# Performance work log

Hardware: AMD Instinct MI355X
Metric: run time of the kernel (lower is better)

The kernel has to match this reference:

```python
import jax, jax.numpy as jnp
import numpy as np

D_MODEL = 1024
N_HEADS = 16
D_K = D_MODEL // N_HEADS
B, S = 4, 2048


def setup_inputs() -> dict:
    key = jax.random.key(0)
    ks = jax.random.split(key, 12)
    scale = 1.0 / np.sqrt(D_MODEL)
    mk = lambda k: (jax.random.uniform(k, (D_MODEL, D_MODEL), jnp.float32, -scale, scale))
    mb = lambda k: (jax.random.uniform(k, (D_MODEL,), jnp.float32, -scale, scale))
    mask = jnp.tril(jnp.ones((S, S), dtype=bool))[None, None, :, :]  # [1,1,S,S] causal
    return {
        "query": jax.random.normal(ks[0], (B, S, D_MODEL), jnp.float32),
        "key": jax.random.normal(ks[1], (B, S, D_MODEL), jnp.float32),
        "value": jax.random.normal(ks[2], (B, S, D_MODEL), jnp.float32),
        "w_q": mk(ks[3]), "b_q": mb(ks[4]),
        "w_k": mk(ks[5]), "b_k": mb(ks[6]),
        "w_v": mk(ks[7]), "b_v": mb(ks[8]),
        "w_o": mk(ks[9]), "b_o": mb(ks[10]),
        "mask": mask,
    }


def _split_heads(x):
    b, s, _ = x.shape
    return x.reshape(b, s, N_HEADS, D_K).transpose(0, 2, 1, 3)  # [B,H,S,Dk]


def reference(query, key, value, w_q, b_q, w_k, b_k, w_v, b_v, w_o, b_o, mask):
    Q = _split_heads(query @ w_q.T + b_q)
    K = _split_heads(key @ w_k.T + b_k)
    V = _split_heads(value @ w_v.T + b_v)
    scores = jnp.einsum("bhqd,bhkd->bhqk", Q, K) / jnp.sqrt(jnp.asarray(D_K, Q.dtype))
    min_val = jnp.finfo(scores.dtype).min
    scores = jnp.where(mask, scores, min_val)
    attn = jax.nn.softmax(scores, axis=-1)
    ctx = jnp.einsum("bhqk,bhkd->bhqd", attn, V)
    ctx = ctx.transpose(0, 2, 1, 3).reshape(query.shape[0], -1, D_MODEL)
    return ctx @ w_o.T + b_o
```

## Files before the change

### kernel.cpp

```cpp
#include <hip/hip_runtime.h>
#include <cstdint>
#include <cstddef>

#define DM 1024
#define NH 16
#define DK 64
#define BB 4
#define SS 2048
#define MROWS (BB*SS)

#define NE_ ((size_t)MROWS * DM)
#define WE_ ((size_t)DM * DM)

typedef __attribute__((ext_vector_type(8))) __bf16 bf16x8;
typedef __attribute__((ext_vector_type(4))) float f32x4;
typedef __attribute__((ext_vector_type(8))) unsigned short ushort8;

#define SCALE_LOG2E 0.18033688011112042f

__device__ __forceinline__ unsigned short f2bf(float f) {
  union { float f; unsigned u; } v; v.f = f;
  unsigned r = v.u + 0x7fffu + ((v.u >> 16) & 1u);
  return (unsigned short)(r >> 16);
}

__device__ __forceinline__ unsigned short f2bf_hw(float f) {
  __bf16 h = (__bf16)f;
  return __builtin_bit_cast(unsigned short, h);
}

__device__ __forceinline__ void async_load16(const void* g, void* l) {
  __builtin_amdgcn_global_load_lds(
      (__attribute__((address_space(1))) void*)(g),
      (__attribute__((address_space(3))) void*)(l),
      16, 0, 0);
}

template<int CTRL>
__device__ __forceinline__ float dppf(float v) {
  int i = __builtin_bit_cast(int, v);
  int r = __builtin_amdgcn_update_dpp(i, i, CTRL, 0xf, 0xf, true);
  return __builtin_bit_cast(float, r);
}
__device__ __forceinline__ float redsum16(float v) {
  v += dppf<0x128>(v);
  v += dppf<0x124>(v);
  v += dppf<0x122>(v);
  v += dppf<0x121>(v);
  return v;
}

struct CvtArgs {
  const float* src[7];
  unsigned short* dst[7];
};

__global__ __launch_bounds__(256)
void cvt_all(CvtArgs a) {
  size_t i = ((size_t)blockIdx.x * 256 + threadIdx.x) * 4;
  int seg; size_t off;
  if (i < 3 * NE_) { seg = (int)(i >> 23); off = i & (NE_ - 1); }
  else { size_t j = i - 3 * NE_; seg = 3 + (int)(j >> 20); off = j & (WE_ - 1); }
  float4 v = *reinterpret_cast<const float4*>(a.src[seg] + off);
  ushort4 o;
  o.x = f2bf(v.x); o.y = f2bf(v.y); o.z = f2bf(v.z); o.w = f2bf(v.w);
  *reinterpret_cast<ushort4*>(a.dst[seg] + off) = o;
}

struct QkvArgs {
  const unsigned short* A[3];
  const unsigned short* W[3];
  const float* bias[3];
  unsigned short* out[3];
};

__global__ __launch_bounds__(256)
void gemm_qkv(QkvArgs qa)
{
  __shared__ __align__(16) unsigned short As[128*32];
  __shared__ __align__(16) unsigned short Bs[128*32];

  const int sel = blockIdx.x >> 3;
  const unsigned short* __restrict__ A  = qa.A[sel];
  const unsigned short* __restrict__ Bw = qa.W[sel];
  const float* __restrict__ bias = qa.bias[sel];
  unsigned short* __restrict__ o = qa.out[sel];
  const float qs = (sel == 0) ? SCALE_LOG2E : 1.0f;

  const int tid  = threadIdx.x;
  const int lane = tid & 63;
  const int wv   = tid >> 6;
  const int wm   = wv >> 1, wn = wv & 1;
  const int gm0  = blockIdx.y * 128;
  const int gn0  = (blockIdx.x & 7) * 128;
  const int lrow = lane & 15;
  const int lk8  = (lane >> 4) * 8;

  f32x4 acc[4][4] = {};

  for (int k0 = 0; k0 < DM; k0 += 32) {
    __syncthreads();
    #pragma unroll
    for (int p = 0; p < 2; ++p) {
      int idx = (p * 256 + tid) * 8;
      int row = idx >> 5;
      int col = idx & 31;
      async_load16(&A [(size_t)(gm0 + row) * DM + k0 + col], &As[idx]);
      async_load16(&Bw[(size_t)(gn0 + row) * DM + k0 + col], &Bs[idx]);
    }
    __syncthreads();

    bf16x8 af[4], bfr[4];
    #pragma unroll
    for (int m = 0; m < 4; ++m)
      af[m] = *reinterpret_cast<const bf16x8*>(&As[(wm*64 + m*16 + lrow)*32 + lk8]);
    #pragma unroll
    for (int n = 0; n < 4; ++n)
      bfr[n] = *reinterpret_cast<const bf16x8*>(&Bs[(wn*64 + n*16 + lrow)*32 + lk8]);
    #pragma unroll
    for (int m = 0; m < 4; ++m)
      #pragma unroll
      for (int n = 0; n < 4; ++n)
        acc[m][n] = __builtin_amdgcn_mfma_f32_16x16x32_bf16(af[m], bfr[n], acc[m][n], 0, 0, 0);
  }

  const int orow = (lane >> 4) * 4;
  const int ocol = lane & 15;
  #pragma unroll
  for (int n = 0; n < 4; ++n) {
    int gn = gn0 + wn*64 + n*16 + ocol;
    float bv = bias[gn] * qs;
    int h = gn >> 6, d = gn & (DK - 1);
    #pragma unroll
    for (int m = 0; m < 4; ++m) {
      #pragma unroll
      for (int r = 0; r < 4; ++r) {
        int gm = gm0 + wm*64 + m*16 + orow + r;
        int b = gm >> 11, s = gm & (SS - 1);
        o[(((size_t)b*NH + h)*SS + s)*DK + d] = f2bf_hw(fmaf(acc[m][n][r], qs, bv));
      }
    }
  }
}

__global__ __launch_bounds__(256)
void gemm_out(const unsigned short* __restrict__ A,
              const unsigned short* __restrict__ Bw,
              const float* __restrict__ bias,
              float* __restrict__ o)
{
  __shared__ __align__(16) unsigned short As[128*32];
  __shared__ __align__(16) unsigned short Bs[128*32];

  const int tid  = threadIdx.x;
  const int lane = tid & 63;
  const int wv   = tid >> 6;
  const int wm   = wv >> 1, wn = wv & 1;
  const int gm0  = blockIdx.y * 128;
  const int gn0  = blockIdx.x * 128;
  const int lrow = lane & 15;
  const int lk8  = (lane >> 4) * 8;

  f32x4 acc[4][4] = {};

  for (int k0 = 0; k0 < DM; k0 += 32) {
    __syncthreads();
    #pragma unroll
    for (int p = 0; p < 2; ++p) {
      int idx = (p * 256 + tid) * 8;
      int row = idx >> 5;
      int col = idx & 31;
      async_load16(&A [(size_t)(gm0 + row) * DM + k0 + col], &As[idx]);
      async_load16(&Bw[(size_t)(gn0 + row) * DM + k0 + col], &Bs[idx]);
    }
    __syncthreads();

    bf16x8 af[4], bfr[4];
    #pragma unroll
    for (int m = 0; m < 4; ++m)
      af[m] = *reinterpret_cast<const bf16x8*>(&As[(wm*64 + m*16 + lrow)*32 + lk8]);
    #pragma unroll
    for (int n = 0; n < 4; ++n)
      bfr[n] = *reinterpret_cast<const bf16x8*>(&Bs[(wn*64 + n*16 + lrow)*32 + lk8]);
    #pragma unroll
    for (int m = 0; m < 4; ++m)
      #pragma unroll
      for (int n = 0; n < 4; ++n)
        acc[m][n] = __builtin_amdgcn_mfma_f32_16x16x32_bf16(af[m], bfr[n], acc[m][n], 0, 0, 0);
  }

  const int orow = (lane >> 4) * 4;
  const int ocol = lane & 15;
  #pragma unroll
  for (int n = 0; n < 4; ++n) {
    int gn = gn0 + wn*64 + n*16 + ocol;
    float bv = bias[gn];
    #pragma unroll
    for (int m = 0; m < 4; ++m)
      #pragma unroll
      for (int r = 0; r < 4; ++r) {
        int gm = gm0 + wm*64 + m*16 + orow + r;
        o[(size_t)gm * DM + gn] = acc[m][n][r] + bv;
      }
  }
}

__global__ __launch_bounds__(256)
void vtrans_kernel(const unsigned short* __restrict__ Vp, unsigned short* __restrict__ VpT) {
  __shared__ unsigned short T[64][72];
  const int bh = blockIdx.x;
  const int st = blockIdx.y;
  const int tid = threadIdx.x;
  #pragma unroll
  for (int p = 0; p < 2; ++p) {
    int i = p*256 + tid;
    int row = i >> 3, c8 = (i & 7) * 8;
    *reinterpret_cast<ushort8*>(&T[row][c8]) =
      *reinterpret_cast<const ushort8*>(&Vp[((size_t)bh*SS + st*64 + row)*DK + c8]);
  }
  __syncthreads();
  #pragma unroll
  for (int p = 0; p < 2; ++p) {
    int i = p*256 + tid;
    int d = i >> 3, s8 = (i & 7) * 8;
    ushort8 o;
    #pragma unroll
    for (int j = 0; j < 8; ++j) o[j] = T[s8 + j][d];
    *reinterpret_cast<ushort8*>(&VpT[((size_t)bh*DK + d)*SS + st*64 + s8]) = o;
  }
}

__global__ __launch_bounds__(512)
void attn_kernel(const unsigned short* __restrict__ Qp,
                 const unsigned short* __restrict__ Kp,
                 const unsigned short* __restrict__ VpT,
                 unsigned short* __restrict__ ctx)
{
  __shared__ __align__(16) unsigned short Kb[2][64*64];
  __shared__ __align__(16) unsigned short Vb[2][64*64];
  __shared__ __align__(16) unsigned short Ps[8][16][72];

  const int tid  = threadIdx.x;
  const int lane = tid & 63;
  const int w    = tid >> 6;
  const int bh   = blockIdx.x;
  const int qt   = gridDim.y - 1 - blockIdx.y;
  const int qb0  = qt * 128;
  const int qw0  = qb0 + w * 16;
  const int lrow = lane & 15;
  const int g0   = lane >> 4;
  const int lk8  = g0 * 8;

  const size_t qbase = ((size_t)bh * SS + qw0 + lrow) * DK;
  bf16x8 aq0 = *reinterpret_cast<const bf16x8*>(&Qp[qbase + lk8]);
  bf16x8 aq1 = *reinterpret_cast<const bf16x8*>(&Qp[qbase + 32 + lk8]);

  f32x4 accc[4] = {};
  float psum[4] = {0.f, 0.f, 0.f, 0.f};

  const int ntiles = 2*qt + 2;
  const int twlast = (qw0 + 15) >> 6;
  const int srow   = tid >> 3;
  const int ssrc   = (tid & 7) ^ (srow & 7);

#define STAGE(B, T) { \
    const int kv0_ = (T) * 64; \
    async_load16(&Kp [((size_t)bh*SS + kv0_ + srow)*DK + ssrc*8], &Kb[B][tid*8]); \
    async_load16(&VpT[((size_t)bh*DK + srow)*SS + kv0_ + ssrc*8], &Vb[B][tid*8]); }

  STAGE(0, 0);

  for (int t = 0; t < ntiles; ++t) {
    const int buf = t & 1;
    asm volatile("s_waitcnt vmcnt(0)" ::: "memory");
    __syncthreads();
    if (t + 1 < ntiles) { if (buf) { STAGE(0, t + 1); } else { STAGE(1, t + 1); } }

    if (t <= twlast) {
      const int kv0 = t * 64;
      const unsigned short* Kc = &Kb[buf][0];
      const unsigned short* Vc = &Vb[buf][0];

      f32x4 sc[4];
      __builtin_amdgcn_s_setprio(1);
      #pragma unroll
      for (int kb = 0; kb < 4; ++kb) {
        const int rk = kb*16 + lrow;
        const int cx = rk & 7;
        bf16x8 bk0 = *reinterpret_cast<const bf16x8*>(&Kc[rk*64 + ((g0    ) ^ cx)*8]);
        bf16x8 bk1 = *reinterpret_cast<const bf16x8*>(&Kc[rk*64 + ((g0 + 4) ^ cx)*8]);
        f32x4 z = {};
        z      = __builtin_amdgcn_mfma_f32_16x16x32_bf16(aq0, bk0, z, 0, 0, 0);
        sc[kb] = __builtin_amdgcn_mfma_f32_16x16x32_bf16(aq1, bk1, z, 0, 0, 0);
      }
      __builtin_amdgcn_s_setprio(0);

      const int qrow0 = qw0 + g0 * 4;
      const bool needmask = (kv0 + 63 > qw0);
      #pragma unroll
      for (int kb = 0; kb < 4; ++kb) {
        const int kvg = kv0 + kb*16 + lrow;
        #pragma unroll
        for (int r = 0; r < 4; ++r) {
          float p = __builtin_amdgcn_exp2f(sc[kb][r]);
          if (needmask && (kvg > qrow0 + r)) p = 0.f;
          sc[kb][r] = p;
          psum[r] += p;
        }
      }

      #pragma unroll
      for (int kb = 0; kb < 4; ++kb)
        #pragma unroll
        for (int r = 0; r < 4; ++r)
          Ps[w][g0*4 + r][kb*16 + lrow] = f2bf_hw(sc[kb][r]);
      asm volatile("s_waitcnt lgkmcnt(0)" ::: "memory");

      bf16x8 pa0 = *reinterpret_cast<const bf16x8*>(&Ps[w][lrow][lk8]);
      bf16x8 pa1 = *reinterpret_cast<const bf16x8*>(&Ps[w][lrow][32 + lk8]);
      __builtin_amdgcn_s_setprio(1);
      #pragma unroll
      for (int db = 0; db < 4; ++db) {
        const int rv = db*16 + lrow;
        const int cv = rv & 7;
        bf16x8 bv0 = *reinterpret_cast<const bf16x8*>(&Vc[rv*64 + ((g0    ) ^ cv)*8]);
        bf16x8 bv1 = *reinterpret_cast<const bf16x8*>(&Vc[rv*64 + ((g0 + 4) ^ cv)*8]);
        accc[db] = __builtin_amdgcn_mfma_f32_16x16x32_bf16(pa0, bv0, accc[db], 0, 0, 0);
        accc[db] = __builtin_amdgcn_mfma_f32_16x16x32_bf16(pa1, bv1, accc[db], 0, 0, 0);
      }
      __builtin_amdgcn_s_setprio(0);
    }
  }

  const int b = bh >> 4, hh = bh & (NH - 1);
  #pragma unroll
  for (int r = 0; r < 4; ++r) {
    int q = qw0 + g0*4 + r;
    float l = redsum16(psum[r]);
    float inv = __builtin_amdgcn_rcpf(l);
    size_t base = ((size_t)b * SS + q) * DM + hh * DK;
    #pragma unroll
    for (int db = 0; db < 4; ++db)
      ctx[base + db*16 + lrow] = f2bf_hw(accc[db][r] * inv);
  }
}

extern "C" void kernel_launch(void* const* d_in, const int* in_sizes, int n_in,
                              void* d_out, int out_size, void* d_ws, size_t ws_size,
                              hipStream_t stream)
{
  const float* q_in = (const float*)d_in[0];
  const float* k_in = (const float*)d_in[1];
  const float* v_in = (const float*)d_in[2];
  const float* w_q  = (const float*)d_in[3];
  const float* b_q  = (const float*)d_in[4];
  const float* w_k  = (const float*)d_in[5];
  const float* b_k  = (const float*)d_in[6];
  const float* w_v  = (const float*)d_in[7];
  const float* b_v  = (const float*)d_in[8];
  const float* w_o  = (const float*)d_in[9];
  const float* b_o  = (const float*)d_in[10];

  char* ws = (char*)d_ws;
  size_t off = 0;
  unsigned short* xb[3];
  unsigned short* wb[4];
  for (int i = 0; i < 3; ++i) { xb[i] = (unsigned short*)(ws + off); off += NE_ * 2; }
  for (int i = 0; i < 4; ++i) { wb[i] = (unsigned short*)(ws + off); off += WE_ * 2; }
  unsigned short* Qp  = (unsigned short*)(ws + off); off += NE_ * 2;
  unsigned short* Kp  = (unsigned short*)(ws + off); off += NE_ * 2;
  unsigned short* Vp  = (unsigned short*)(ws + off); off += NE_ * 2;
  unsigned short* ctx = (unsigned short*)(ws + off); off += NE_ * 2;
  unsigned short* VpT = xb[2];

  CvtArgs ca;
  ca.src[0] = q_in; ca.dst[0] = xb[0];
  ca.src[1] = k_in; ca.dst[1] = xb[1];
  ca.src[2] = v_in; ca.dst[2] = xb[2];
  ca.src[3] = w_q;  ca.dst[3] = wb[0];
  ca.src[4] = w_k;  ca.dst[4] = wb[1];
  ca.src[5] = w_v;  ca.dst[5] = wb[2];
  ca.src[6] = w_o;  ca.dst[6] = wb[3];
  const int cvt_blocks = (int)((3*NE_ + 4*WE_) / 1024);
  cvt_all<<<cvt_blocks, 256, 0, stream>>>(ca);

  QkvArgs qa;
  qa.A[0] = xb[0]; qa.W[0] = wb[0]; qa.bias[0] = b_q; qa.out[0] = Qp;
  qa.A[1] = xb[1]; qa.W[1] = wb[1]; qa.bias[1] = b_k; qa.out[1] = Kp;
  qa.A[2] = xb[2]; qa.W[2] = wb[2]; qa.bias[2] = b_v; qa.out[2] = Vp;
  gemm_qkv<<<dim3(24, MROWS/128), 256, 0, stream>>>(qa);

  vtrans_kernel<<<dim3(BB*NH, SS/64), 256, 0, stream>>>(Vp, VpT);

  attn_kernel<<<dim3(BB*NH, SS/128), 512, 0, stream>>>(Qp, Kp, VpT, ctx);

  gemm_out<<<dim3(DM/128, MROWS/128), 256, 0, stream>>>(ctx, wb[3], b_o, (float*)d_out);
}
```

Baseline: 200.4 us.

## Double-buffer GEMM LDS tiles, remap workgroups for XCD locality, raise MFMA priority

Both projection GEMMs now use two LDS buffers per operand, so the async global loads for the next K tile are issued while MFMAs run on the current tile, and one barrier per iteration is removed. Workgroup IDs are permuted so consecutive blocks land on the same XCD, aiming for better L2 reuse of A and W tiles. s_setprio is raised around the MFMA block. LDS use per block doubles, which may reduce occupancy, and the single vmcnt(0) wait limits how much load latency is hidden.

```diff
diff --git a/kernel.cpp b/kernel.cpp
--- a/kernel.cpp
+++ b/kernel.cpp
@@ -77,10 +77,14 @@
 __global__ __launch_bounds__(256)
 void gemm_qkv(QkvArgs qa)
 {
-  __shared__ __align__(16) unsigned short As[128*32];
-  __shared__ __align__(16) unsigned short Bs[128*32];
-
-  const int sel = blockIdx.x >> 3;
+  __shared__ __align__(16) unsigned short As[2][128*32];
+  __shared__ __align__(16) unsigned short Bs[2][128*32];
+
+  int wgid = blockIdx.x + blockIdx.y * 24;
+  wgid = (wgid & 7) * 192 + (wgid >> 3);
+  const int bx = wgid % 24, by = wgid / 24;
+
+  const int sel = bx >> 3;
   const unsigned short* __restrict__ A  = qa.A[sel];
   const unsigned short* __restrict__ Bw = qa.W[sel];
   const float* __restrict__ bias = qa.bias[sel];
@@ -91,37 +95,45 @@
   const int lane = tid & 63;
   const int wv   = tid >> 6;
   const int wm   = wv >> 1, wn = wv & 1;
-  const int gm0  = blockIdx.y * 128;
-  const int gn0  = (blockIdx.x & 7) * 128;
+  const int gm0  = by * 128;
+  const int gn0  = (bx & 7) * 128;
   const int lrow = lane & 15;
   const int lk8  = (lane >> 4) * 8;
 
   f32x4 acc[4][4] = {};
 
-  for (int k0 = 0; k0 < DM; k0 += 32) {
+#define GSTAGE(B, K0) { \
+    _Pragma("unroll") \
+    for (int p_ = 0; p_ < 2; ++p_) { \
+      int idx_ = (p_ * 256 + tid) * 8; \
+      int row_ = idx_ >> 5; \
+      int col_ = idx_ & 31; \
+      async_load16(&A [(size_t)(gm0 + row_) * DM + (K0) + col_], &As[B][idx_]); \
+      async_load16(&Bw[(size_t)(gn0 + row_) * DM + (K0) + col_], &Bs[B][idx_]); \
+    } }
+
+  GSTAGE(0, 0);
+
+  for (int kt = 0; kt < 32; ++kt) {
+    const int buf = kt & 1;
+    asm volatile("s_waitcnt vmcnt(0)" ::: "memory");
     __syncthreads();
-    #pragma unroll
-    for (int p = 0; p < 2; ++p) {
-      int idx = (p * 256 + tid) * 8;
-      int row = idx >> 5;
-      int col = idx & 31;
-      async_load16(&A [(size_t)(gm0 + row) * DM + k0 + col], &As[idx]);
-      async_load16(&Bw[(size_t)(gn0 + row) * DM + k0 + col], &Bs[idx]);
-    }
-    __syncthreads();
+    if (kt + 1 < 32) { if (buf) { GSTAGE(0, (kt+1)*32); } else { GSTAGE(1, (kt+1)*32); } }
 
     bf16x8 af[4], bfr[4];
     #pragma unroll
     for (int m = 0; m < 4; ++m)
-      af[m] = *reinterpret_cast<const bf16x8*>(&As[(wm*64 + m*16 + lrow)*32 + lk8]);
+      af[m] = *reinterpret_cast<const bf16x8*>(&As[buf][(wm*64 + m*16 + lrow)*32 + lk8]);
     #pragma unroll
     for (int n = 0; n < 4; ++n)
-      bfr[n] = *reinterpret_cast<const bf16x8*>(&Bs[(wn*64 + n*16 + lrow)*32 + lk8]);
+      bfr[n] = *reinterpret_cast<const bf16x8*>(&Bs[buf][(wn*64 + n*16 + lrow)*32 + lk8]);
+    __builtin_amdgcn_s_setprio(1);
     #pragma unroll
     for (int m = 0; m < 4; ++m)
       #pragma unroll
       for (int n = 0; n < 4; ++n)
         acc[m][n] = __builtin_amdgcn_mfma_f32_16x16x32_bf16(af[m], bfr[n], acc[m][n], 0, 0, 0);
+    __builtin_amdgcn_s_setprio(0);
   }
 
   const int orow = (lane >> 4) * 4;
@@ -149,44 +161,46 @@
               const float* __restrict__ bias,
               float* __restrict__ o)
 {
-  __shared__ __align__(16) unsigned short As[128*32];
-  __shared__ __align__(16) unsigned short Bs[128*32];
+  __shared__ __align__(16) unsigned short As[2][128*32];
+  __shared__ __align__(16) unsigned short Bs[2][128*32];
+
+  int wgid = blockIdx.x + blockIdx.y * 8;
+  wgid = (wgid & 7) * 64 + (wgid >> 3);
+  const int bx = wgid & 7, by = wgid >> 3;
 
   const int tid  = threadIdx.x;
   const int lane = tid & 63;
   const int wv   = tid >> 6;
   const int wm   = wv >> 1, wn = wv & 1;
-  const int gm0  = blockIdx.y * 128;
-  const int gn0  = blockIdx.x * 128;
+  const int gm0  = by * 128;
+  const int gn0  = bx * 128;
   const int lrow = lane & 15;
   const int lk8  = (lane >> 4) * 8;
 
   f32x4 acc[4][4] = {};
 
-  for (int k0 = 0; k0 < DM; k0 += 32) {
+  GSTAGE(0, 0);
+
+  for (int kt = 0; kt < 32; ++kt) {
+    const int buf = kt & 1;
+    asm volatile("s_waitcnt vmcnt(0)" ::: "memory");
     __syncthreads();
-    #pragma unroll
-    for (int p = 0; p < 2; ++p) {
-      int idx = (p * 256 + tid) * 8;
-      int row = idx >> 5;
-      int col = idx & 31;
-      async_load16(&A [(size_t)(gm0 + row) * DM + k0 + col], &As[idx]);
-      async_load16(&Bw[(size_t)(gn0 + row) * DM + k0 + col], &Bs[idx]);
-    }
-    __syncthreads();
+    if (kt + 1 < 32) { if (buf) { GSTAGE(0, (kt+1)*32); } else { GSTAGE(1, (kt+1)*32); } }
 
     bf16x8 af[4], bfr[4];
     #pragma unroll
     for (int m = 0; m < 4; ++m)
-      af[m] = *reinterpret_cast<const bf16x8*>(&As[(wm*64 + m*16 + lrow)*32 + lk8]);
+      af[m] = *reinterpret_cast<const bf16x8*>(&As[buf][(wm*64 + m*16 + lrow)*32 + lk8]);
     #pragma unroll
     for (int n = 0; n < 4; ++n)
-      bfr[n] = *reinterpret_cast<const bf16x8*>(&Bs[(wn*64 + n*16 + lrow)*32 + lk8]);
+      bfr[n] = *reinterpret_cast<const bf16x8*>(&Bs[buf][(wn*64 + n*16 + lrow)*32 + lk8]);
+    __builtin_amdgcn_s_setprio(1);
     #pragma unroll
     for (int m = 0; m < 4; ++m)
       #pragma unroll
       for (int n = 0; n < 4; ++n)
         acc[m][n] = __builtin_amdgcn_mfma_f32_16x16x32_bf16(af[m], bfr[n], acc[m][n], 0, 0, 0);
+    __builtin_amdgcn_s_setprio(0);
   }
 
   const int orow = (lane >> 4) * 4;
```

New measurement: 187.8 us. 1.07x faster.
